# Kernel optimization log

Hardware: AMD Instinct MI355X
Metric: run time of the kernel (lower is better)

## Reference

```python
import math
import jax, jax.numpy as jnp
import numpy as np

H_CYCLES, L_CYCLES = 3, 2
STD = 0.02


def setup_inputs() -> dict:
    key = jax.random.key(0)
    ks = jax.random.split(key, 11)
    D, nh, mult, V, T, B = 512, 8, 64, 8192, 512, 4
    N = mult * D // nh
    def nrm(k, shape):
        return jax.random.normal(k, shape, jnp.float32) * STD
    return {
        "idx": jax.random.randint(ks[0], (B, T), 0, V),
        "embed_w": nrm(ks[1], (V, D)),
        "h_enc": nrm(ks[2], (nh, D, N)),
        "h_enc_v": nrm(ks[3], (nh, D, N)),
        "h_dec": nrm(ks[4], (nh * N, D)),
        "l_enc": nrm(ks[5], (nh, D, N)),
        "l_enc_v": nrm(ks[6], (nh, D, N)),
        "l_dec": nrm(ks[7], (nh * N, D)),
        "lm_head": nrm(ks[8], (D, V)),
        "h_init": nrm(ks[9], (D,)),
        "l_init": nrm(ks[10], (D,)),
    }


def _ln(x, eps=1e-5):
    # LayerNorm without affine params (elementwise_affine=False)
    m = jnp.mean(x, axis=-1, keepdims=True)
    v = jnp.var(x, axis=-1, keepdims=True)
    return (x - m) * jax.lax.rsqrt(v + eps)


def _rope_tables(T, N):
    # freqs with even-quantized exponent, angles wrapped mod 1 then scaled by 2*pi
    q = jnp.floor(jnp.arange(N, dtype=jnp.float32) / 2.0) * 2.0
    freqs = 1.0 / jnp.power(2.0 ** 16, q / N) / (2.0 * math.pi)
    phases = jnp.arange(T, dtype=jnp.float32)[:, None] * freqs[None, :]
    ang = (phases % 1.0) * (2.0 * math.pi)
    return jnp.cos(ang), jnp.sin(ang)  # each (T, N)


def _rope(v, cos, sin):
    # v: (B, nh, T, N); interleaved rotation as in torch stack/view trick
    v_rot = jnp.stack((-v[..., 1::2], v[..., ::2]), axis=-1).reshape(v.shape)
    return v * cos + v_rot * sin


def _attn(x_sparse, Vmat, cos, sin):
    # x_sparse: (B, nh, T, N); Vmat: (B, T, D)
    N = x_sparse.shape[-1]
    T = x_sparse.shape[-2]
    QR = _rope(x_sparse, cos, sin)
    scores = jnp.einsum('bhtn,bhsn->bhts', QR, QR) * (N ** -0.5)
    mask = jnp.tril(jnp.ones((T, T), dtype=bool), k=-1)  # strict lower triangle
    scores = jnp.where(mask, scores, 0.0)
    return jnp.einsum('bhts,bsd->bhtd', scores, Vmat)  # (B, nh, T, D)


def _block(x, inj, enc, enc_v, dec, cos, sin):
    # x, inj: (B, 1, T, D)
    B, _, T, D = x.shape
    nh, _, N = enc.shape
    xi = _ln(x + inj)[:, 0]  # (B, T, D)
    x_sparse = jax.nn.relu(jnp.einsum('btd,hdn->bhtn', xi, enc))
    yKV = _ln(_attn(x_sparse, xi, cos, sin))  # (B, nh, T, D)
    y_sparse = jax.nn.relu(jnp.einsum('bhtd,hdn->bhtn', yKV, enc_v))
    xy = (x_sparse * y_sparse).transpose(0, 2, 1, 3).reshape(B, 1, T, nh * N)
    y = _ln(xy @ dec)  # (B, 1, T, D)
    return _ln(x + y)


def reference(idx, embed_w, h_enc, h_enc_v, h_dec, l_enc, l_enc_v, l_dec,
              lm_head, h_init, l_init):
    B, T = idx.shape
    D = embed_w.shape[1]
    N = l_enc.shape[-1]
    cos, sin = _rope_tables(T, N)
    inp = _ln(embed_w[idx])[:, None]  # (B, 1, T, D)
    z_H = jnp.broadcast_to(h_init, (B, 1, T, D))
    z_L = jnp.broadcast_to(l_init, (B, 1, T, D))
    for h in range(H_CYCLES):
        for l in range(L_CYCLES):
            if not (h == H_CYCLES - 1 and l == L_CYCLES - 1):
                z_L = _block(z_L, z_H + inp, l_enc, l_enc_v, l_dec, cos, sin)
        if h < H_CYCLES - 1:
            z_H = _block(z_H, z_L, h_enc, h_enc_v, h_dec, cos, sin)
    z_L = _block(z_L, z_H + inp, l_enc, l_enc_v, l_dec, cos, sin)
    z_H = _block(z_H, z_L, h_enc, h_enc_v, h_dec, cos, sin)
    logits = z_H[:, 0] @ lm_head  # (B, T, vocab)
    return logits
```

## Files before the change

kernel.cpp:

```cpp
#include <hip/hip_runtime.h>

typedef _Float16 f16;
typedef __attribute__((ext_vector_type(8))) _Float16 f16x8;
typedef __attribute__((ext_vector_type(4))) float f32x4;
typedef __attribute__((ext_vector_type(4))) int i32x4;

#define D_  512
#define NH_ 8
#define NS_ 4096
#define TT_ 512
#define BB_ 4
#define VV_ 8192
#define HN_ 32768
#define BT_ 2048


__device__ __forceinline__ void gl16(const void* g, void* l) {
  __builtin_amdgcn_global_load_lds((const __attribute__((address_space(1))) void*)g,
                                   (__attribute__((address_space(3))) void*)l, 16, 0, 0);
}

__device__ __forceinline__ void gemm_core(const f16* __restrict__ A, const f16* __restrict__ B,
    int lda, int ldb, int nk, char* As, char* Bs, f32x4 acc[4][4]) {
  int tid = threadIdx.x;
  int l = tid & 63, wid = tid >> 6;
  int wm = wid >> 1, wn = wid & 1;
  int row0 = tid >> 3, g0 = tid & 7;
  for (int kt = 0; kt < nk; ++kt) {
    __syncthreads();
#pragma unroll
    for (int it = 0; it < 4; ++it) {
      int row = row0 + 32 * it;
      int gs = g0 ^ (row & 7);
      int wb = (wid * 64 + it * 256) * 16;
      gl16(A + (size_t)row * lda + gs * 8, As + wb);
      gl16(B + (size_t)row * ldb + gs * 8, Bs + wb);
    }
    __syncthreads();
    A += 64; B += 64;
#pragma unroll
    for (int kh = 0; kh < 2; ++kh) {
      f16x8 af[4], bfr[4];
#pragma unroll
      for (int m = 0; m < 4; ++m) {
        int row = wm * 64 + m * 16 + (l & 15);
        af[m] = *(const f16x8*)(As + row * 128 + ((kh * 64 + (l >> 4) * 16) ^ ((row & 7) << 4)));
      }
#pragma unroll
      for (int n = 0; n < 4; ++n) {
        int row = wn * 64 + n * 16 + (l & 15);
        bfr[n] = *(const f16x8*)(Bs + row * 128 + ((kh * 64 + (l >> 4) * 16) ^ ((row & 7) << 4)));
      }
#pragma unroll
      for (int m = 0; m < 4; ++m)
#pragma unroll
        for (int n = 0; n < 4; ++n)
          acc[m][n] = __builtin_amdgcn_mfma_f32_16x16x32_f16(af[m], bfr[n], acc[m][n], 0, 0, 0);
    }
  }
}


__global__ __launch_bounds__(256, 4) void k_gemm_xs(
    const f16* __restrict__ xi, const f16* __restrict__ encT,
    const f16* __restrict__ csT, f16* __restrict__ qr) {
  __shared__ i32x4 As4[1024], Bs4[1024];
  int bid = blockIdx.x;
  int swz = (bid & 7) * 512 + (bid >> 3);
  int mt = swz & 15, nt = (swz >> 4) & 31, h = swz >> 9;
  const f16* A = xi + (size_t)mt * 128 * D_;
  const f16* B = encT + ((size_t)h * NS_ + nt * 128) * D_;
  f32x4 acc[4][4] = {};
  gemm_core(A, B, D_, D_, D_ / 64, (char*)As4, (char*)Bs4, acc);
  int l = threadIdx.x & 63, wid = threadIdx.x >> 6;
  int wm = wid >> 1, wn = wid & 1;
  int r04 = (l >> 4) * 4, c0 = l & 15;
  int b = (mt * 128) >> 9;
  int tbase = (mt * 128) & (TT_ - 1);
#pragma unroll
  for (int m = 0; m < 4; ++m)
#pragma unroll
    for (int n = 0; n < 4; ++n)
#pragma unroll
      for (int r = 0; r < 4; ++r) {
        int row = wm * 64 + m * 16 + r04 + r;
        int col = wn * 64 + n * 16 + c0;
        int t = tbase + row;
        int nn = nt * 128 + col;
        float xsv = fmaxf(acc[m][n][r], 0.f);
        float prt = __shfl_xor(xsv, 1);
        int ci = 2 * (t * NS_ + nn);
        float c = (float)csT[ci], s = (float)csT[ci + 1];
        float qv = xsv * c + ((nn & 1) ? prt : -prt) * s;
        size_t o = (((size_t)b * NH_ + h) * TT_ + t) * NS_ + nn;
        qr[o] = (f16)qv;
      }
}

__global__ __launch_bounds__(256, 4) void k_gemm_scores(
    const f16* __restrict__ qr, f16* __restrict__ scores) {
  __shared__ i32x4 As4[1024], Bs4[1024];
  int bid = blockIdx.x;
  int swz = (bid & 7) * 40 + (bid >> 3);
  int x = swz % 10, z = swz / 10;
  int mt = (x >= 6) ? 3 : (x >= 3) ? 2 : (x >= 1) ? 1 : 0;
  int nt = x - mt * (mt + 1) / 2;
  const f16* base = qr + (size_t)z * TT_ * NS_;
  const f16* A = base + (size_t)mt * 128 * NS_;
  const f16* B = base + (size_t)nt * 128 * NS_;
  f32x4 acc[4][4] = {};
  gemm_core(A, B, NS_, NS_, NS_ / 64, (char*)As4, (char*)Bs4, acc);
  int l = threadIdx.x & 63, wid = threadIdx.x >> 6;
  int wm = wid >> 1, wn = wid & 1;
  int r04 = (l >> 4) * 4, c0 = l & 15;
  f16* outp = scores + (size_t)z * TT_ * TT_;
#pragma unroll
  for (int m = 0; m < 4; ++m)
#pragma unroll
    for (int n = 0; n < 4; ++n)
#pragma unroll
      for (int r = 0; r < 4; ++r) {
        int t = mt * 128 + wm * 64 + m * 16 + r04 + r;
        int s_ = nt * 128 + wn * 64 + n * 16 + c0;
        float v = (t > s_) ? acc[m][n][r] * 0.015625f : 0.f;
        outp[(size_t)t * TT_ + s_] = (f16)v;
      }
}

__global__ __launch_bounds__(256, 4) void k_gemm_attn(
    const f16* __restrict__ scores, const f16* __restrict__ xiT, f16* __restrict__ attn) {
  __shared__ i32x4 As4[1024], Bs4[1024];
  int bid = blockIdx.x;
  int swz = (bid & 7) * 64 + (bid >> 3);
  int mt = swz & 3, ntd = (swz >> 2) & 3, z = swz >> 4;
  int b = z >> 3;
  const f16* A = scores + (size_t)z * TT_ * TT_ + (size_t)mt * 128 * TT_;
  const f16* B = xiT + (size_t)b * D_ * TT_ + (size_t)ntd * 128 * TT_;
  f32x4 acc[4][4] = {};
  gemm_core(A, B, TT_, TT_, 2 * mt + 2, (char*)As4, (char*)Bs4, acc);
  int l = threadIdx.x & 63, wid = threadIdx.x >> 6;
  int wm = wid >> 1, wn = wid & 1;
  int r04 = (l >> 4) * 4, c0 = l & 15;
#pragma unroll
  for (int m = 0; m < 4; ++m)
#pragma unroll
    for (int n = 0; n < 4; ++n)
#pragma unroll
      for (int r = 0; r < 4; ++r) {
        int t = mt * 128 + wm * 64 + m * 16 + r04 + r;
        int d = ntd * 128 + wn * 64 + n * 16 + c0;
        attn[((size_t)z * TT_ + t) * D_ + d] = (f16)acc[m][n][r];
      }
}

__global__ __launch_bounds__(256, 4) void k_gemm_xy(
    const f16* __restrict__ ykv, const f16* __restrict__ encvT,
    const f16* __restrict__ csT, f16* __restrict__ qrxy) {
  __shared__ i32x4 As4[1024], Bs4[1024];
  int bid = blockIdx.x;
  int xcd = bid & 7, k = bid >> 3;
  int h = xcd, b = k >> 7, nt = (k >> 2) & 31, mt = k & 3;
  int z = b * NH_ + h;
  const f16* A = ykv + (size_t)z * TT_ * D_ + (size_t)mt * 128 * D_;
  const f16* B = encvT + ((size_t)h * NS_ + nt * 128) * D_;
  f32x4 acc[4][4] = {};
  gemm_core(A, B, D_, D_, D_ / 64, (char*)As4, (char*)Bs4, acc);
  int l = threadIdx.x & 63, wid = threadIdx.x >> 6;
  int wm = wid >> 1, wn = wid & 1;
  int r04 = (l >> 4) * 4, c0 = l & 15;
#pragma unroll
  for (int m = 0; m < 4; ++m)
#pragma unroll
    for (int n = 0; n < 4; ++n)
#pragma unroll
      for (int r = 0; r < 4; ++r) {
        int t = mt * 128 + wm * 64 + m * 16 + r04 + r;
        int nn = nt * 128 + wn * 64 + n * 16 + c0;
        float ys = fmaxf(acc[m][n][r], 0.f);
        size_t o = ((size_t)z * TT_ + t) * NS_ + nn;
        float qv = (float)qrxy[o];
        float prt = __shfl_xor(qv, 1);
        int ci = 2 * (t * NS_ + nn);
        float c = (float)csT[ci], s = (float)csT[ci + 1];
        float xsv = (nn & 1) ? (qv * c - prt * s) : (qv * c + prt * s);
        qrxy[o] = (f16)(xsv * ys);
      }
}

__global__ __launch_bounds__(256, 4) void k_gemm_ydec(
    const f16* __restrict__ xy, const f16* __restrict__ decT, f16* __restrict__ ypart) {
  __shared__ i32x4 As4[1024], Bs4[1024];
  int bid = blockIdx.x;
  int swz = (bid & 7) * 64 + (bid >> 3);
  int mt = swz & 15, nt = (swz >> 4) & 3, kz = swz >> 6;
  int b = mt >> 2, t0 = (mt & 3) * 128;
  const f16* A = xy + ((size_t)(b * NH_ + kz) * TT_ + t0) * NS_;
  const f16* B = decT + (size_t)nt * 128 * HN_ + (size_t)kz * NS_;
  f32x4 acc[4][4] = {};
  gemm_core(A, B, NS_, HN_, NS_ / 64, (char*)As4, (char*)Bs4, acc);
  int l = threadIdx.x & 63, wid = threadIdx.x >> 6;
  int wm = wid >> 1, wn = wid & 1;
  int r04 = (l >> 4) * 4, c0 = l & 15;
  f16* outp = ypart + (size_t)kz * BT_ * D_;
#pragma unroll
  for (int m = 0; m < 4; ++m)
#pragma unroll
    for (int n = 0; n < 4; ++n)
#pragma unroll
      for (int r = 0; r < 4; ++r) {
        int R = mt * 128 + wm * 64 + m * 16 + r04 + r;
        int c = nt * 128 + wn * 64 + n * 16 + c0;
        outp[(size_t)R * D_ + c] = (f16)acc[m][n][r];
      }
}

__global__ __launch_bounds__(256, 4) void k_gemm_logits(
    const f16* __restrict__ zbf, const f16* __restrict__ lmT, float* __restrict__ outp) {
  __shared__ i32x4 As4[1024], Bs4[1024];
  int bid = blockIdx.x;
  int swz = (bid & 7) * 128 + (bid >> 3);
  int mt = swz & 15, nt = swz >> 4;
  const f16* A = zbf + (size_t)mt * 128 * D_;
  const f16* B = lmT + (size_t)nt * 128 * D_;
  f32x4 acc[4][4] = {};
  gemm_core(A, B, D_, D_, D_ / 64, (char*)As4, (char*)Bs4, acc);
  int l = threadIdx.x & 63, wid = threadIdx.x >> 6;
  int wm = wid >> 1, wn = wid & 1;
  int r04 = (l >> 4) * 4, c0 = l & 15;
#pragma unroll
  for (int m = 0; m < 4; ++m)
#pragma unroll
    for (int n = 0; n < 4; ++n)
#pragma unroll
      for (int r = 0; r < 4; ++r) {
        int R = mt * 128 + wm * 64 + m * 16 + r04 + r;
        int v = nt * 128 + wn * 64 + n * 16 + c0;
        outp[(size_t)R * VV_ + v] = acc[m][n][r];
      }
}


__device__ __forceinline__ float wave_sum(float v) {
#pragma unroll
  for (int o = 32; o > 0; o >>= 1) v += __shfl_xor(v, o);
  return v;
}

__global__ __launch_bounds__(256) void k_tables(f16* __restrict__ csT) {
  int i = blockIdx.x * 256 + threadIdx.x;
  int t = i >> 12, n = i & (NS_ - 1);
  float q = (float)(n & ~1);
  float freq = exp2f(-16.f * q / 4096.f) * 0.15915494309189535f;
  float ph = (float)t * freq;
  ph -= floorf(ph);
  float ang = ph * 6.283185307179586f;
  csT[2 * i]     = (f16)cosf(ang);
  csT[2 * i + 1] = (f16)sinf(ang);
}

__global__ void k_transpose(const float* __restrict__ in, f16* __restrict__ outp, int R, int C) {
  __shared__ float tile[32][33];
  size_t mo = (size_t)blockIdx.z * R * C;
  in += mo; outp += mo;
  int c0 = blockIdx.x * 32, r0 = blockIdx.y * 32;
#pragma unroll
  for (int i = threadIdx.y; i < 32; i += 8)
    tile[i][threadIdx.x] = in[(size_t)(r0 + i) * C + c0 + threadIdx.x];
  __syncthreads();
#pragma unroll
  for (int i = threadIdx.y; i < 32; i += 8)
    outp[(size_t)(c0 + i) * R + r0 + threadIdx.x] = (f16)tile[threadIdx.x][i];
}

__global__ __launch_bounds__(256) void k_embed_ln(const int* __restrict__ idx,
    const float* __restrict__ emb, f16* __restrict__ inp) {
  int r = blockIdx.x * 4 + (threadIdx.x >> 6);
  int lane = threadIdx.x & 63;
  const float* e = emb + (size_t)idx[r] * D_ + lane * 8;
  f32x4 e0 = *(const f32x4*)e;
  f32x4 e1 = *(const f32x4*)(e + 4);
  float v[8];
#pragma unroll
  for (int i = 0; i < 4; ++i) { v[i] = e0[i]; v[i + 4] = e1[i]; }
  float s = 0.f;
#pragma unroll
  for (int i = 0; i < 8; ++i) s += v[i];
  float mean = wave_sum(s) * (1.f / 512.f);
  float q = 0.f;
#pragma unroll
  for (int i = 0; i < 8; ++i) { v[i] -= mean; q += v[i] * v[i]; }
  float rs = rsqrtf(wave_sum(q) * (1.f / 512.f) + 1e-5f);
  f16x8 ov;
#pragma unroll
  for (int i = 0; i < 8; ++i) ov[i] = (f16)(v[i] * rs);
  *(f16x8*)(inp + (size_t)r * D_ + lane * 8) = ov;
}

__global__ __launch_bounds__(256) void k_init(const float* __restrict__ hi,
    const float* __restrict__ li, f16* __restrict__ zH, f16* __restrict__ zL) {
  size_t i = (size_t)blockIdx.x * 256 + threadIdx.x;
  zH[i] = (f16)hi[i & (D_ - 1)];
  zL[i] = (f16)li[i & (D_ - 1)];
}

__global__ __launch_bounds__(256) void k_ln_xi(const f16* __restrict__ x,
    const f16* __restrict__ a1, const f16* __restrict__ a2,
    f16* __restrict__ xi, f16* __restrict__ xiT) {
  int r = blockIdx.x * 4 + (threadIdx.x >> 6);
  int lane = threadIdx.x & 63;
  size_t o = (size_t)r * D_ + lane * 8;
  f16x8 xv = *(const f16x8*)(x + o);
  f16x8 av = *(const f16x8*)(a1 + o);
  float v[8];
#pragma unroll
  for (int i = 0; i < 8; ++i) v[i] = (float)xv[i] + (float)av[i];
  if (a2) {
    f16x8 bv = *(const f16x8*)(a2 + o);
#pragma unroll
    for (int i = 0; i < 8; ++i) v[i] += (float)bv[i];
  }
  float s = 0.f;
#pragma unroll
  for (int i = 0; i < 8; ++i) s += v[i];
  float mean = wave_sum(s) * (1.f / 512.f);
  float q = 0.f;
#pragma unroll
  for (int i = 0; i < 8; ++i) { v[i] -= mean; q += v[i] * v[i]; }
  float rs = rsqrtf(wave_sum(q) * (1.f / 512.f) + 1e-5f);
  f16x8 ov;
#pragma unroll
  for (int i = 0; i < 8; ++i) ov[i] = (f16)(v[i] * rs);
  *(f16x8*)(xi + o) = ov;
  int b = r >> 9, t = r & (TT_ - 1);
  int d0 = lane * 8;
#pragma unroll
  for (int i = 0; i < 8; ++i)
    xiT[((size_t)b * D_ + d0 + i) * TT_ + t] = ov[i];
}

__global__ __launch_bounds__(256) void k_ln_rows(const f16* __restrict__ in, f16* __restrict__ outp) {
  int r = blockIdx.x * 4 + (threadIdx.x >> 6);
  int lane = threadIdx.x & 63;
  size_t o = (size_t)r * D_ + lane * 8;
  f16x8 xv = *(const f16x8*)(in + o);
  float v[8];
#pragma unroll
  for (int i = 0; i < 8; ++i) v[i] = (float)xv[i];
  float s = 0.f;
#pragma unroll
  for (int i = 0; i < 8; ++i) s += v[i];
  float mean = wave_sum(s) * (1.f / 512.f);
  float q = 0.f;
#pragma unroll
  for (int i = 0; i < 8; ++i) { v[i] -= mean; q += v[i] * v[i]; }
  float rs = rsqrtf(wave_sum(q) * (1.f / 512.f) + 1e-5f);
  f16x8 ov;
#pragma unroll
  for (int i = 0; i < 8; ++i) ov[i] = (f16)(v[i] * rs);
  *(f16x8*)(outp + o) = ov;
}

__global__ __launch_bounds__(256) void k_ln_y_out(const f16* __restrict__ ypart,
    f16* __restrict__ z) {
  int r = blockIdx.x * 4 + (threadIdx.x >> 6);
  int lane = threadIdx.x & 63;
  size_t o = (size_t)r * D_ + lane * 8;
  float v[8] = {};
#pragma unroll
  for (int k = 0; k < 8; ++k) {
    f16x8 p = *(const f16x8*)(ypart + (size_t)k * BT_ * D_ + o);
#pragma unroll
    for (int i = 0; i < 8; ++i) v[i] += (float)p[i];
  }
  float s = 0.f;
#pragma unroll
  for (int i = 0; i < 8; ++i) s += v[i];
  float mean = wave_sum(s) * (1.f / 512.f);
  float q = 0.f;
#pragma unroll
  for (int i = 0; i < 8; ++i) { v[i] -= mean; q += v[i] * v[i]; }
  float rs = rsqrtf(wave_sum(q) * (1.f / 512.f) + 1e-5f);
  f16x8 zv = *(const f16x8*)(z + o);
#pragma unroll
  for (int i = 0; i < 8; ++i) v[i] = (float)zv[i] + v[i] * rs;
  s = 0.f;
#pragma unroll
  for (int i = 0; i < 8; ++i) s += v[i];
  mean = wave_sum(s) * (1.f / 512.f);
  q = 0.f;
#pragma unroll
  for (int i = 0; i < 8; ++i) { v[i] -= mean; q += v[i] * v[i]; }
  rs = rsqrtf(wave_sum(q) * (1.f / 512.f) + 1e-5f);
  f16x8 ov;
#pragma unroll
  for (int i = 0; i < 8; ++i) ov[i] = (f16)(v[i] * rs);
  *(f16x8*)(z + o) = ov;
}


extern "C" void kernel_launch(void* const* d_in, const int* in_sizes, int n_in,
                              void* d_out, int out_size, void* d_ws, size_t ws_size,
                              hipStream_t stream) {
  (void)in_sizes; (void)n_in; (void)out_size;
  const int*   idx    = (const int*)  d_in[0];
  const float* emb    = (const float*)d_in[1];
  const float* h_enc  = (const float*)d_in[2];
  const float* h_encv = (const float*)d_in[3];
  const float* h_dec  = (const float*)d_in[4];
  const float* l_enc  = (const float*)d_in[5];
  const float* l_encv = (const float*)d_in[6];
  const float* l_dec  = (const float*)d_in[7];
  const float* lm     = (const float*)d_in[8];
  const float* h_init = (const float*)d_in[9];
  const float* l_init = (const float*)d_in[10];
  float* out = (float*)d_out;

  bool resident = ws_size >= ((size_t)352 << 20);

  char* w = (char*)d_ws;
  size_t off = 0;
  auto alloc = [&](size_t n) { void* p = w + off; off += (n + 255) & ~(size_t)255; return p; };
  f16* csT = (f16*)alloc(8388608);
  f16 *encT[2], *encvT[2], *decT[2], *lmT;
  if (resident) {
    for (int s = 0; s < 2; ++s) {
      encT[s]  = (f16*)alloc(33554432);
      encvT[s] = (f16*)alloc(33554432);
      decT[s]  = (f16*)alloc(33554432);
    }
    lmT = (f16*)alloc(8388608);
  } else {
    encT[0]  = encT[1]  = (f16*)alloc(33554432);
    encvT[0] = encvT[1] = (f16*)alloc(33554432);
    decT[0]  = decT[1]  = (f16*)alloc(33554432);
    lmT = encT[0];
  }
  f16* inp    = (f16*)alloc(2097152);
  f16* zH     = (f16*)alloc(2097152);
  f16* zL     = (f16*)alloc(2097152);
  f16* xi_bf  = (f16*)alloc(2097152);
  f16* xiT_bf = (f16*)alloc(2097152);
  f16* qrxy   = (f16*)alloc(134217728);

  f16* scoresB = (f16*)d_out;
  f16* attnP   = (f16*)((char*)d_out + 16777216);
  f16* ypart   = attnP;
  f16* ykv     = (f16*)((char*)d_out + 33554432);

  dim3 tb(32, 8);
  auto transpose_set = [&](int sel) {
    const float* e  = sel ? h_enc  : l_enc;
    const float* ev = sel ? h_encv : l_encv;
    const float* dc = sel ? h_dec  : l_dec;
    k_transpose<<<dim3(128, 16, 8), tb, 0, stream>>>(e,  encT[sel],  512, 4096);
    k_transpose<<<dim3(128, 16, 8), tb, 0, stream>>>(ev, encvT[sel], 512, 4096);
    k_transpose<<<dim3(16, 1024, 1), tb, 0, stream>>>(dc, decT[sel], 32768, 512);
  };

  k_tables<<<8192, 256, 0, stream>>>(csT);
  k_embed_ln<<<512, 256, 0, stream>>>(idx, emb, inp);
  k_init<<<4096, 256, 0, stream>>>(h_init, l_init, zH, zL);
  if (resident) {
    transpose_set(0);
    transpose_set(1);
    k_transpose<<<dim3(256, 16, 1), tb, 0, stream>>>(lm, lmT, 512, 8192);
  }

  int cur = -1;
  auto setw = [&](int sel) {
    if (resident || cur == sel) { cur = sel; return; }
    cur = sel;
    transpose_set(sel);
  };

  auto run_block = [&](f16* zx, const f16* a1, const f16* a2, int s) {
    k_ln_xi<<<512, 256, 0, stream>>>(zx, a1, a2, xi_bf, xiT_bf);
    k_gemm_xs<<<4096, 256, 0, stream>>>(xi_bf, encT[s], csT, qrxy);
    k_gemm_scores<<<320, 256, 0, stream>>>(qrxy, scoresB);
    k_gemm_attn<<<512, 256, 0, stream>>>(scoresB, xiT_bf, attnP);
    k_ln_rows<<<4096, 256, 0, stream>>>(attnP, ykv);
    k_gemm_xy<<<4096, 256, 0, stream>>>(ykv, encvT[s], csT, qrxy);
    k_gemm_ydec<<<512, 256, 0, stream>>>(qrxy, decT[s], ypart);
    k_ln_y_out<<<512, 256, 0, stream>>>(ypart, zx);
  };

  for (int i = 0; i < 3; ++i) {
    setw(0);
    run_block(zL, inp, zH, 0);
    run_block(zL, inp, zH, 0);
    setw(1);
    run_block(zH, zL, (const f16*)nullptr, 1);
  }
  if (!resident)
    k_transpose<<<dim3(256, 16, 1), tb, 0, stream>>>(lm, lmT, 512, 8192);
  k_gemm_logits<<<1024, 256, 0, stream>>>(zH, lmT, out);
}
```

Baseline: 3.986 ms.

## Swap GEMM operands so epilogue writes contiguous vectorized 4-element stores

```diff
diff --git a/kernel.cpp b/kernel.cpp
--- a/kernel.cpp
+++ b/kernel.cpp
@@ -1,6 +1,7 @@
 #include <hip/hip_runtime.h>
 
 typedef _Float16 f16;
+typedef __attribute__((ext_vector_type(4))) _Float16 f16x4;
 typedef __attribute__((ext_vector_type(8))) _Float16 f16x8;
 typedef __attribute__((ext_vector_type(4))) float f32x4;
 typedef __attribute__((ext_vector_type(4))) int i32x4;
@@ -68,8 +69,8 @@
   int bid = blockIdx.x;
   int swz = (bid & 7) * 512 + (bid >> 3);
   int mt = swz & 15, nt = (swz >> 4) & 31, h = swz >> 9;
-  const f16* A = xi + (size_t)mt * 128 * D_;
-  const f16* B = encT + ((size_t)h * NS_ + nt * 128) * D_;
+  const f16* A = encT + ((size_t)h * NS_ + nt * 128) * D_;
+  const f16* B = xi + (size_t)mt * 128 * D_;
   f32x4 acc[4][4] = {};
   gemm_core(A, B, D_, D_, D_ / 64, (char*)As4, (char*)Bs4, acc);
   int l = threadIdx.x & 63, wid = threadIdx.x >> 6;
@@ -80,21 +81,20 @@
 #pragma unroll
   for (int m = 0; m < 4; ++m)
 #pragma unroll
-    for (int n = 0; n < 4; ++n)
-#pragma unroll
-      for (int r = 0; r < 4; ++r) {
-        int row = wm * 64 + m * 16 + r04 + r;
-        int col = wn * 64 + n * 16 + c0;
-        int t = tbase + row;
-        int nn = nt * 128 + col;
-        float xsv = fmaxf(acc[m][n][r], 0.f);
-        float prt = __shfl_xor(xsv, 1);
-        int ci = 2 * (t * NS_ + nn);
-        float c = (float)csT[ci], s = (float)csT[ci + 1];
-        float qv = xsv * c + ((nn & 1) ? prt : -prt) * s;
-        size_t o = (((size_t)b * NH_ + h) * TT_ + t) * NS_ + nn;
-        qr[o] = (f16)qv;
-      }
+    for (int n = 0; n < 4; ++n) {
+      int nn0 = nt * 128 + wm * 64 + m * 16 + r04;
+      int t = tbase + wn * 64 + n * 16 + c0;
+      f16x8 cs = *(const f16x8*)(csT + 2 * ((size_t)t * NS_ + nn0));
+      f32x4 a = acc[m][n];
+      float x0 = fmaxf(a[0], 0.f), x1 = fmaxf(a[1], 0.f);
+      float x2 = fmaxf(a[2], 0.f), x3 = fmaxf(a[3], 0.f);
+      f16x4 q;
+      q[0] = (f16)(x0 * (float)cs[0] - x1 * (float)cs[1]);
+      q[1] = (f16)(x1 * (float)cs[2] + x0 * (float)cs[3]);
+      q[2] = (f16)(x2 * (float)cs[4] - x3 * (float)cs[5]);
+      q[3] = (f16)(x3 * (float)cs[6] + x2 * (float)cs[7]);
+      *(f16x4*)(qr + (((size_t)b * NH_ + h) * TT_ + t) * NS_ + nn0) = q;
+    }
 }
 
 __global__ __launch_bounds__(256, 4) void k_gemm_scores(
@@ -106,8 +106,8 @@
   int mt = (x >= 6) ? 3 : (x >= 3) ? 2 : (x >= 1) ? 1 : 0;
   int nt = x - mt * (mt + 1) / 2;
   const f16* base = qr + (size_t)z * TT_ * NS_;
-  const f16* A = base + (size_t)mt * 128 * NS_;
-  const f16* B = base + (size_t)nt * 128 * NS_;
+  const f16* A = base + (size_t)nt * 128 * NS_;
+  const f16* B = base + (size_t)mt * 128 * NS_;
   f32x4 acc[4][4] = {};
   gemm_core(A, B, NS_, NS_, NS_ / 64, (char*)As4, (char*)Bs4, acc);
   int l = threadIdx.x & 63, wid = threadIdx.x >> 6;
@@ -117,14 +117,16 @@
 #pragma unroll
   for (int m = 0; m < 4; ++m)
 #pragma unroll
-    for (int n = 0; n < 4; ++n)
-#pragma unroll
-      for (int r = 0; r < 4; ++r) {
-        int t = mt * 128 + wm * 64 + m * 16 + r04 + r;
-        int s_ = nt * 128 + wn * 64 + n * 16 + c0;
-        float v = (t > s_) ? acc[m][n][r] * 0.015625f : 0.f;
-        outp[(size_t)t * TT_ + s_] = (f16)v;
-      }
+    for (int n = 0; n < 4; ++n) {
+      int s0 = nt * 128 + wm * 64 + m * 16 + r04;
+      int t = mt * 128 + wn * 64 + n * 16 + c0;
+      f32x4 a = acc[m][n];
+      f16x4 q;
+#pragma unroll
+      for (int r = 0; r < 4; ++r)
+        q[r] = (f16)((t > s0 + r) ? a[r] * 0.015625f : 0.f);
+      *(f16x4*)(outp + (size_t)t * TT_ + s0) = q;
+    }
 }
 
 __global__ __launch_bounds__(256, 4) void k_gemm_attn(
@@ -134,8 +136,8 @@
   int swz = (bid & 7) * 64 + (bid >> 3);
   int mt = swz & 3, ntd = (swz >> 2) & 3, z = swz >> 4;
   int b = z >> 3;
-  const f16* A = scores + (size_t)z * TT_ * TT_ + (size_t)mt * 128 * TT_;
-  const f16* B = xiT + (size_t)b * D_ * TT_ + (size_t)ntd * 128 * TT_;
+  const f16* A = xiT + (size_t)b * D_ * TT_ + (size_t)ntd * 128 * TT_;
+  const f16* B = scores + (size_t)z * TT_ * TT_ + (size_t)mt * 128 * TT_;
   f32x4 acc[4][4] = {};
   gemm_core(A, B, TT_, TT_, 2 * mt + 2, (char*)As4, (char*)Bs4, acc);
   int l = threadIdx.x & 63, wid = threadIdx.x >> 6;
@@ -144,13 +146,15 @@
 #pragma unroll
   for (int m = 0; m < 4; ++m)
 #pragma unroll
-    for (int n = 0; n < 4; ++n)
-#pragma unroll
-      for (int r = 0; r < 4; ++r) {
-        int t = mt * 128 + wm * 64 + m * 16 + r04 + r;
-        int d = ntd * 128 + wn * 64 + n * 16 + c0;
-        attn[((size_t)z * TT_ + t) * D_ + d] = (f16)acc[m][n][r];
-      }
+    for (int n = 0; n < 4; ++n) {
+      int d0 = ntd * 128 + wm * 64 + m * 16 + r04;
+      int t = mt * 128 + wn * 64 + n * 16 + c0;
+      f32x4 a = acc[m][n];
+      f16x4 q;
+#pragma unroll
+      for (int r = 0; r < 4; ++r) q[r] = (f16)a[r];
+      *(f16x4*)(attn + ((size_t)z * TT_ + t) * D_ + d0) = q;
+    }
 }
 
 __global__ __launch_bounds__(256, 4) void k_gemm_xy(
@@ -161,8 +165,8 @@
   int xcd = bid & 7, k = bid >> 3;
   int h = xcd, b = k >> 7, nt = (k >> 2) & 31, mt = k & 3;
   int z = b * NH_ + h;
-  const f16* A = ykv + (size_t)z * TT_ * D_ + (size_t)mt * 128 * D_;
-  const f16* B = encvT + ((size_t)h * NS_ + nt * 128) * D_;
+  const f16* A = encvT + ((size_t)h * NS_ + nt * 128) * D_;
+  const f16* B = ykv + (size_t)z * TT_ * D_ + (size_t)mt * 128 * D_;
   f32x4 acc[4][4] = {};
   gemm_core(A, B, D_, D_, D_ / 64, (char*)As4, (char*)Bs4, acc);
   int l = threadIdx.x & 63, wid = threadIdx.x >> 6;
@@ -171,20 +175,26 @@
 #pragma unroll
   for (int m = 0; m < 4; ++m)
 #pragma unroll
-    for (int n = 0; n < 4; ++n)
-#pragma unroll
-      for (int r = 0; r < 4; ++r) {
-        int t = mt * 128 + wm * 64 + m * 16 + r04 + r;
-        int nn = nt * 128 + wn * 64 + n * 16 + c0;
-        float ys = fmaxf(acc[m][n][r], 0.f);
-        size_t o = ((size_t)z * TT_ + t) * NS_ + nn;
-        float qv = (float)qrxy[o];
-        float prt = __shfl_xor(qv, 1);
-        int ci = 2 * (t * NS_ + nn);
-        float c = (float)csT[ci], s = (float)csT[ci + 1];
-        float xsv = (nn & 1) ? (qv * c - prt * s) : (qv * c + prt * s);
-        qrxy[o] = (f16)(xsv * ys);
-      }
+    for (int n = 0; n < 4; ++n) {
+      int nn0 = nt * 128 + wm * 64 + m * 16 + r04;
+      int t = mt * 128 + wn * 64 + n * 16 + c0;
+      size_t o = ((size_t)z * TT_ + t) * NS_ + nn0;
+      f16x4 q4 = *(const f16x4*)(qrxy + o);
+      f16x8 cs = *(const f16x8*)(csT + 2 * ((size_t)t * NS_ + nn0));
+      f32x4 a = acc[m][n];
+      float qe0 = (float)q4[0], qo0 = (float)q4[1];
+      float qe1 = (float)q4[2], qo1 = (float)q4[3];
+      float xe0 = qe0 * (float)cs[0] + qo0 * (float)cs[1];
+      float xo0 = qo0 * (float)cs[2] - qe0 * (float)cs[3];
+      float xe1 = qe1 * (float)cs[4] + qo1 * (float)cs[5];
+      float xo1 = qo1 * (float)cs[6] - qe1 * (float)cs[7];
+      f16x4 outv;
+      outv[0] = (f16)(xe0 * fmaxf(a[0], 0.f));
+      outv[1] = (f16)(xo0 * fmaxf(a[1], 0.f));
+      outv[2] = (f16)(xe1 * fmaxf(a[2], 0.f));
+      outv[3] = (f16)(xo1 * fmaxf(a[3], 0.f));
+      *(f16x4*)(qrxy + o) = outv;
+    }
 }
 
 __global__ __launch_bounds__(256, 4) void k_gemm_ydec(
@@ -194,10 +204,10 @@
   int swz = (bid & 7) * 64 + (bid >> 3);
   int mt = swz & 15, nt = (swz >> 4) & 3, kz = swz >> 6;
   int b = mt >> 2, t0 = (mt & 3) * 128;
-  const f16* A = xy + ((size_t)(b * NH_ + kz) * TT_ + t0) * NS_;
-  const f16* B = decT + (size_t)nt * 128 * HN_ + (size_t)kz * NS_;
+  const f16* A = decT + (size_t)nt * 128 * HN_ + (size_t)kz * NS_;
+  const f16* B = xy + ((size_t)(b * NH_ + kz) * TT_ + t0) * NS_;
   f32x4 acc[4][4] = {};
-  gemm_core(A, B, NS_, HN_, NS_ / 64, (char*)As4, (char*)Bs4, acc);
+  gemm_core(A, B, HN_, NS_, NS_ / 64, (char*)As4, (char*)Bs4, acc);
   int l = threadIdx.x & 63, wid = threadIdx.x >> 6;
   int wm = wid >> 1, wn = wid & 1;
   int r04 = (l >> 4) * 4, c0 = l & 15;
@@ -205,13 +215,15 @@
 #pragma unroll
   for (int m = 0; m < 4; ++m)
 #pragma unroll
-    for (int n = 0; n < 4; ++n)
-#pragma unroll
-      for (int r = 0; r < 4; ++r) {
-        int R = mt * 128 + wm * 64 + m * 16 + r04 + r;
-        int c = nt * 128 + wn * 64 + n * 16 + c0;
-        outp[(size_t)R * D_ + c] = (f16)acc[m][n][r];
-      }
+    for (int n = 0; n < 4; ++n) {
+      int cc0 = nt * 128 + wm * 64 + m * 16 + r04;
+      int R = mt * 128 + wn * 64 + n * 16 + c0;
+      f32x4 a = acc[m][n];
+      f16x4 q;
+#pragma unroll
+      for (int r = 0; r < 4; ++r) q[r] = (f16)a[r];
+      *(f16x4*)(outp + (size_t)R * D_ + cc0) = q;
+    }
 }
 
 __global__ __launch_bounds__(256, 4) void k_gemm_logits(
@@ -220,8 +232,8 @@
   int bid = blockIdx.x;
   int swz = (bid & 7) * 128 + (bid >> 3);
   int mt = swz & 15, nt = swz >> 4;
-  const f16* A = zbf + (size_t)mt * 128 * D_;
-  const f16* B = lmT + (size_t)nt * 128 * D_;
+  const f16* A = lmT + (size_t)nt * 128 * D_;
+  const f16* B = zbf + (size_t)mt * 128 * D_;
   f32x4 acc[4][4] = {};
   gemm_core(A, B, D_, D_, D_ / 64, (char*)As4, (char*)Bs4, acc);
   int l = threadIdx.x & 63, wid = threadIdx.x >> 6;
@@ -230,13 +242,11 @@
 #pragma unroll
   for (int m = 0; m < 4; ++m)
 #pragma unroll
-    for (int n = 0; n < 4; ++n)
-#pragma unroll
-      for (int r = 0; r < 4; ++r) {
-        int R = mt * 128 + wm * 64 + m * 16 + r04 + r;
-        int v = nt * 128 + wn * 64 + n * 16 + c0;
-        outp[(size_t)R * VV_ + v] = acc[m][n][r];
-      }
+    for (int n = 0; n < 4; ++n) {
+      int v0 = nt * 128 + wm * 64 + m * 16 + r04;
+      int R = mt * 128 + wn * 64 + n * 16 + c0;
+      *(f32x4*)(outp + (size_t)R * VV_ + v0) = acc[m][n];
+    }
 }
 
 
```

Result: slower. 4.760 ms (+19.4%).
